# Kernel tuning notes

Measured on AMD Instinct MI355X. Metric: run time of the kernel, lower is better.

## Reference

```python
import jax, jax.numpy as jnp
import numpy as np

B, S, D = 2, 2048, 1024
H, HD = 16, 64

def setup_inputs() -> dict:
    key = jax.random.key(0)
    ks = jax.random.split(key, 5)
    scale = 1.0 / np.sqrt(D)
    x = jax.random.normal(ks[0], (B, S, D), dtype=jnp.float32)
    wq = jax.random.normal(ks[1], (D, H * HD), dtype=jnp.float32) * scale
    wk = jax.random.normal(ks[2], (D, H * HD), dtype=jnp.float32) * scale
    wv = jax.random.normal(ks[3], (D, H * HD), dtype=jnp.float32) * scale
    wo = jax.random.normal(ks[4], (H * HD, D), dtype=jnp.float32) * scale
    zeros = jnp.zeros((H * HD,), dtype=jnp.float32)
    return {"x": x, "wq": wq, "bq": zeros, "wk": wk, "bk": zeros,
            "wv": wv, "bv": zeros, "wo": wo, "bo": jnp.zeros((D,), jnp.float32)}

def reference(x, wq, bq, wk, bk, wv, bv, wo, bo):
    b, s, _ = x.shape
    att_scale = HD ** -0.5
    # QKV projections -> [b, h, s, hd]
    q = (x @ wq + bq).reshape(b, s, H, HD).transpose(0, 2, 1, 3)
    k = (x @ wk + bk).reshape(b, s, H, HD).transpose(0, 2, 1, 3)
    v = (x @ wv + bv).reshape(b, s, H, HD).transpose(0, 2, 1, 3)
    scores = jnp.einsum('bhqd,bhkd->bhqk', q, k) * att_scale
    weights = jax.nn.softmax(scores, axis=-1)
    out = jnp.einsum('bhqk,bhkd->bhqd', weights, v)
    out = out.transpose(0, 2, 1, 3).reshape(b, s, H * HD)
    return out @ wo + bo
```

## Files before the change

### kernel.cpp

```cpp
#include <hip/hip_runtime.h>
#include <hip/hip_bf16.h>

#define B_  2
#define S_  2048
#define D_  1024
#define H_  16
#define HD_ 64
#define M_  (B_*S_)

using bf16x8 = __attribute__((ext_vector_type(8))) short;
using f32x4  = __attribute__((ext_vector_type(4))) float;
using f32x16 = __attribute__((ext_vector_type(16))) float;
using u32x4  = __attribute__((ext_vector_type(4))) unsigned int;
using uint2v = __attribute__((ext_vector_type(2))) unsigned int;

static __device__ __forceinline__ ushort f2bf(float f) {
    __hip_bfloat16 h = __float2bfloat16(f);
    return *reinterpret_cast<ushort*>(&h);
}
static __device__ __forceinline__ float max3f(float a, float b, float c) {
    return fmaxf(fmaxf(a, b), c);
}
static __device__ __forceinline__ float fexp2(float x) {
#if __has_builtin(__builtin_amdgcn_exp2f)
    return __builtin_amdgcn_exp2f(x);
#else
    return exp2f(x);
#endif
}
static __device__ __forceinline__ unsigned int pack_bf16(float p0, float p1) {
    unsigned int a = __float_as_uint(p0), b = __float_as_uint(p1);
    a += 0x7fffu + ((a >> 16) & 1u);
    b += 0x7fffu + ((b >> 16) & 1u);
    return (a >> 16) | (b & 0xffff0000u);
}

#define GLDS16(gp, lp) __builtin_amdgcn_global_load_lds( \
    (const __attribute__((address_space(1))) void*)(gp), \
    (__attribute__((address_space(3))) void*)(lp), 16, 0, 0)

__global__ void convert_f32_bf16(const float* __restrict__ src, ushort* __restrict__ dst, int n) {
    int i = (blockIdx.x * blockDim.x + threadIdx.x) * 4;
    if (i < n) {
        float4 v = *reinterpret_cast<const float4*>(src + i);
        ushort4 o;
        o.x = f2bf(v.x); o.y = f2bf(v.y); o.z = f2bf(v.z); o.w = f2bf(v.w);
        *reinterpret_cast<ushort4*>(dst + i) = o;
    }
}

__global__ void transpose_f32_to_bf16(const float* __restrict__ src, ushort* __restrict__ dst,
                                      int R, int C) {
    __shared__ float t[32][33];
    int c0 = blockIdx.x * 32, r0 = blockIdx.y * 32;
    int tx = threadIdx.x, ty = threadIdx.y;
    #pragma unroll
    for (int i = 0; i < 4; i++)
        t[ty + i*8][tx] = src[(size_t)(r0 + ty + i*8) * C + c0 + tx];
    __syncthreads();
    #pragma unroll
    for (int i = 0; i < 4; i++)
        dst[(size_t)(c0 + ty + i*8) * R + r0 + tx] = f2bf(t[tx][ty + i*8]);
}

__global__ void transpose_v(const ushort* __restrict__ src, ushort* __restrict__ dst) {
    __shared__ ushort t[64][72];
    int bh = blockIdx.y, s0 = blockIdx.x * 64;
    #pragma unroll
    for (int p = 0; p < 2; p++) {
        int idx = threadIdx.x + p * 256;
        int r = idx >> 3, cu = (idx & 7) * 8;
        uint4 v = *reinterpret_cast<const uint4*>(src + (size_t)bh * 131072 + (size_t)(s0 + r) * 64 + cu);
        ushort tmp[8];
        *reinterpret_cast<uint4*>(tmp) = v;
        #pragma unroll
        for (int j = 0; j < 8; j++) t[cu + j][r] = tmp[j];
    }
    __syncthreads();
    #pragma unroll
    for (int p = 0; p < 2; p++) {
        int idx = threadIdx.x + p * 256;
        int r = idx >> 3, cu = (idx & 7) * 8;
        *reinterpret_cast<uint4*>(dst + (size_t)bh * 131072 + (size_t)r * S_ + s0 + cu) =
            *reinterpret_cast<uint4*>(&t[r][cu]);
    }
}

template<int MODE>
__launch_bounds__(256, 2)
__global__ void gemm_bt(const ushort* __restrict__ A, const ushort* __restrict__ Bt,
                        int Mdim, int Ndim, int Kdim,
                        ushort* __restrict__ qout, ushort* __restrict__ kout, ushort* __restrict__ vout,
                        const float* __restrict__ bq, const float* __restrict__ bk, const float* __restrict__ bv,
                        float* __restrict__ out, const float* __restrict__ bias)
{
    __shared__ __align__(16) ushort As[128][32];
    __shared__ __align__(16) ushort Bs[128][32];
    const int tid  = threadIdx.x;
    const int lane = tid & 63, wave = tid >> 6;
    const int wm = wave & 1, wn = wave >> 1;
    const int m0 = blockIdx.y * 128, n0 = blockIdx.x * 128;
    const int g = lane >> 4, c = lane & 15;

    f32x4 acc[4][4];
    #pragma unroll
    for (int i = 0; i < 4; i++)
        #pragma unroll
        for (int j = 0; j < 4; j++) acc[i][j] = (f32x4){0.f, 0.f, 0.f, 0.f};

    const int lrow = lane >> 2;
    const int lcol = (lane & 3) * 8;

    for (int kt = 0; kt < Kdim; kt += 32) {
        #pragma unroll
        for (int p = 0; p < 2; p++) {
            int ch = wave + p * 4;
            GLDS16(A  + (size_t)(m0 + ch*16 + lrow) * Kdim + kt + lcol, &As[ch*16][0]);
            GLDS16(Bt + (size_t)(n0 + ch*16 + lrow) * Kdim + kt + lcol, &Bs[ch*16][0]);
        }
        __syncthreads();
        bf16x8 af[4], bfr[4];
        #pragma unroll
        for (int t = 0; t < 4; t++) {
            af[t]  = *reinterpret_cast<const bf16x8*>(&As[wm*64 + t*16 + c][g*8]);
            bfr[t] = *reinterpret_cast<const bf16x8*>(&Bs[wn*64 + t*16 + c][g*8]);
        }
        #pragma unroll
        for (int i = 0; i < 4; i++)
            #pragma unroll
            for (int j = 0; j < 4; j++)
                acc[i][j] = __builtin_amdgcn_mfma_f32_16x16x32_bf16(af[i], bfr[j], acc[i][j], 0, 0, 0);
        __syncthreads();
    }

    const float qscale = 0.125f * 1.4426950408889634f;
    #pragma unroll
    for (int i = 0; i < 4; i++) {
      #pragma unroll
      for (int j = 0; j < 4; j++) {
        #pragma unroll
        for (int r = 0; r < 4; r++) {
            int row = m0 + wm*64 + i*16 + g*4 + r;
            int col = n0 + wn*64 + j*16 + c;
            float v = acc[i][j][r];
            if (MODE == 0) {
                int which = col >> 10;
                int cc = col & 1023;
                int b = row >> 11, s = row & 2047;
                int h = cc >> 6, hd = cc & 63;
                size_t dst = (((size_t)(b*H_ + h)) * S_ + s) * HD_ + hd;
                if (which == 0)      qout[dst] = f2bf((v + bq[cc]) * qscale);
                else if (which == 1) kout[dst] = f2bf(v + bk[cc]);
                else                 vout[dst] = f2bf(v + bv[cc]);
            } else {
                out[(size_t)row * Ndim + col] = v + bias[col];
            }
        }
      }
    }
}

__launch_bounds__(512, 4)
__global__ void attn_kernel(const ushort* __restrict__ Q, const ushort* __restrict__ K,
                            const ushort* __restrict__ Vt, ushort* __restrict__ O)
{
    __shared__ __align__(16) ushort Ks[2][2][64][64];
    __shared__ __align__(16) ushort Vs[2][2][64][64];
    const int tid = threadIdx.x, lane = tid & 63, w = tid >> 6;
    const int grp = w >> 2, wq4 = w & 3;
    const int q31 = lane & 31, hi = lane >> 5, x7 = lane & 7;

    int lin = blockIdx.x + gridDim.x * blockIdx.y;
    int xcd = lin & 7, idx = lin >> 3;
    int bh = xcd * 4 + (idx & 3);
    int qb = idx >> 2;
    const int q0 = qb * 128;
    const int kt_base = grp * 1024;
    const ushort* Kp = K  + (size_t)bh * S_ * HD_;
    const ushort* Vp = Vt + (size_t)bh * HD_ * S_;

    bf16x8 qf[4];
    #pragma unroll
    for (int c4 = 0; c4 < 4; c4++)
        qf[c4] = *reinterpret_cast<const bf16x8*>(
            Q + (size_t)bh * S_ * HD_ + (size_t)(q0 + wq4*32 + q31) * HD_ + c4*16 + hi*8);

    f32x16 acc0, acc1;
    #pragma unroll
    for (int r = 0; r < 16; r++) { acc0[r] = 0.f; acc1[r] = 0.f; }
    float m_i = -INFINITY, l_i = 0.f;

    const int srow  = lane >> 3;
    const int sslot = (lane & 7) ^ srow;
    const ushort* kg = Kp + (size_t)srow * HD_ + sslot * 8;
    const ushort* vg = Vp + (size_t)srow * S_  + sslot * 8;

    auto stage = [&](int buf, int kt) {
        #pragma unroll
        for (int p = 0; p < 2; p++) {
            int ch = wq4 + p * 4;
            GLDS16(kg + (size_t)(kt + ch*8) * HD_, &Ks[grp][buf][ch*8][0]);
            GLDS16(vg + (size_t)(ch*8) * S_ + kt,  &Vs[grp][buf][ch*8][0]);
        }
    };

    auto softmax_pack = [&](const f32x16& st, bf16x8& pf0, bf16x8& pf1) {
        float g0 = max3f(st[0],  st[1],  st[2]);
        float g1 = max3f(st[3],  st[4],  st[5]);
        float g2 = max3f(st[6],  st[7],  st[8]);
        float g3 = max3f(st[9],  st[10], st[11]);
        float g4 = max3f(st[12], st[13], st[14]);
        float pm = fmaxf(max3f(g0, g1, g2), max3f(g3, g4, st[15]));
#if __has_builtin(__builtin_amdgcn_permlane32_swap)
        {
            uint2v r = __builtin_amdgcn_permlane32_swap(__float_as_uint(pm), __float_as_uint(pm), false, false);
            pm = fmaxf(__uint_as_float(r.x), __uint_as_float(r.y));
        }
#else
        pm = fmaxf(pm, __shfl_xor(pm, 32));
#endif
        if (__any(pm > m_i + 8.f)) {
            float mnew = fmaxf(m_i, pm);
            float al = fexp2(m_i - mnew);
            l_i *= al;
            #pragma unroll
            for (int r = 0; r < 16; r++) { acc0[r] *= al; acc1[r] *= al; }
            m_i = mnew;
        }
        float rs = 0.f;
        unsigned int dd[8];
        #pragma unroll
        for (int r2 = 0; r2 < 8; r2++) {
            float p0 = fexp2(st[r2*2]     - m_i);
            float p1 = fexp2(st[r2*2 + 1] - m_i);
            rs += p0 + p1;
            dd[r2] = pack_bf16(p0, p1);
        }
#if __has_builtin(__builtin_amdgcn_permlane32_swap)
        {
            uint2v r = __builtin_amdgcn_permlane32_swap(__float_as_uint(rs), __float_as_uint(rs), false, false);
            rs = __uint_as_float(r.x) + __uint_as_float(r.y);
        }
#else
        rs += __shfl_xor(rs, 32);
#endif
        l_i += rs;
        u32x4 t0, t1;
#if __has_builtin(__builtin_amdgcn_permlane32_swap)
        {
            uint2v s02 = __builtin_amdgcn_permlane32_swap(dd[0], dd[2], false, false);
            uint2v s13 = __builtin_amdgcn_permlane32_swap(dd[1], dd[3], false, false);
            uint2v s46 = __builtin_amdgcn_permlane32_swap(dd[4], dd[6], false, false);
            uint2v s57 = __builtin_amdgcn_permlane32_swap(dd[5], dd[7], false, false);
            t0 = (u32x4){s02.x, s13.x, s02.y, s13.y};
            t1 = (u32x4){s46.x, s57.x, s46.y, s57.y};
        }
#else
        {
            unsigned int ee[8];
            #pragma unroll
            for (int r2 = 0; r2 < 8; r2++)
                ee[r2] = (unsigned int)__shfl_xor((int)dd[r2], 32);
            t0 = (u32x4){ hi ? ee[2] : dd[0], hi ? ee[3] : dd[1],
                          hi ? dd[2] : ee[0], hi ? dd[3] : ee[1] };
            t1 = (u32x4){ hi ? ee[6] : dd[4], hi ? ee[7] : dd[5],
                          hi ? dd[6] : ee[4], hi ? dd[7] : ee[5] };
        }
#endif
        pf0 = *reinterpret_cast<bf16x8*>(&t0);
        pf1 = *reinterpret_cast<bf16x8*>(&t1);
    };

    auto compute64 = [&](int buf) {
        const ushort (*ks)[64] = Ks[grp][buf];
        const ushort (*vs)[64] = Vs[grp][buf];
        f32x16 st0, st1;
        #pragma unroll
        for (int r = 0; r < 16; r++) { st0[r] = 0.f; st1[r] = 0.f; }
        __builtin_amdgcn_s_setprio(1);
        #pragma unroll
        for (int c4 = 0; c4 < 4; c4++) {
            bf16x8 kf = *reinterpret_cast<const bf16x8*>(&ks[q31][((c4*2 + hi) ^ x7) * 8]);
            st0 = __builtin_amdgcn_mfma_f32_32x32x16_bf16(kf, qf[c4], st0, 0, 0, 0);
        }
        #pragma unroll
        for (int c4 = 0; c4 < 4; c4++) {
            bf16x8 kf = *reinterpret_cast<const bf16x8*>(&ks[32 + q31][((c4*2 + hi) ^ x7) * 8]);
            st1 = __builtin_amdgcn_mfma_f32_32x32x16_bf16(kf, qf[c4], st1, 0, 0, 0);
        }
        __builtin_amdgcn_s_setprio(0);

        bf16x8 pf0, pf1;
        softmax_pack(st0, pf0, pf1);
        {
            bf16x8 vf0 = *reinterpret_cast<const bf16x8*>(&vs[q31]     [((0 + hi) ^ x7) * 8]);
            bf16x8 vf1 = *reinterpret_cast<const bf16x8*>(&vs[q31]     [((2 + hi) ^ x7) * 8]);
            bf16x8 vf2 = *reinterpret_cast<const bf16x8*>(&vs[32 + q31][((0 + hi) ^ x7) * 8]);
            bf16x8 vf3 = *reinterpret_cast<const bf16x8*>(&vs[32 + q31][((2 + hi) ^ x7) * 8]);
            __builtin_amdgcn_s_setprio(1);
            acc0 = __builtin_amdgcn_mfma_f32_32x32x16_bf16(vf0, pf0, acc0, 0, 0, 0);
            acc0 = __builtin_amdgcn_mfma_f32_32x32x16_bf16(vf1, pf1, acc0, 0, 0, 0);
            acc1 = __builtin_amdgcn_mfma_f32_32x32x16_bf16(vf2, pf0, acc1, 0, 0, 0);
            acc1 = __builtin_amdgcn_mfma_f32_32x32x16_bf16(vf3, pf1, acc1, 0, 0, 0);
            __builtin_amdgcn_s_setprio(0);
        }
        softmax_pack(st1, pf0, pf1);
        {
            bf16x8 vf0 = *reinterpret_cast<const bf16x8*>(&vs[q31]     [((4 + hi) ^ x7) * 8]);
            bf16x8 vf1 = *reinterpret_cast<const bf16x8*>(&vs[q31]     [((6 + hi) ^ x7) * 8]);
            bf16x8 vf2 = *reinterpret_cast<const bf16x8*>(&vs[32 + q31][((4 + hi) ^ x7) * 8]);
            bf16x8 vf3 = *reinterpret_cast<const bf16x8*>(&vs[32 + q31][((6 + hi) ^ x7) * 8]);
            __builtin_amdgcn_s_setprio(1);
            acc0 = __builtin_amdgcn_mfma_f32_32x32x16_bf16(vf0, pf0, acc0, 0, 0, 0);
            acc0 = __builtin_amdgcn_mfma_f32_32x32x16_bf16(vf1, pf1, acc0, 0, 0, 0);
            acc1 = __builtin_amdgcn_mfma_f32_32x32x16_bf16(vf2, pf0, acc1, 0, 0, 0);
            acc1 = __builtin_amdgcn_mfma_f32_32x32x16_bf16(vf3, pf1, acc1, 0, 0, 0);
            __builtin_amdgcn_s_setprio(0);
        }
    };

    stage(0, kt_base);
    __syncthreads();
    #pragma unroll 1
    for (int it = 0; it < 15; ++it) {
        stage((it & 1) ^ 1, kt_base + (it + 1) * 64);
        compute64(it & 1);
        __syncthreads();
    }
    compute64(1);

    __syncthreads();
    float* fb = (wq4 < 2) ? reinterpret_cast<float*>(&Ks[0][0][0][0])
                          : reinterpret_cast<float*>(&Vs[0][0][0][0]);
    const int slot = ((wq4 & 1) * 64 + lane) * 35;
    if (grp == 1) {
        #pragma unroll
        for (int r = 0; r < 16; r++) { fb[slot + r] = acc0[r]; fb[slot + 16 + r] = acc1[r]; }
        fb[slot + 32] = m_i;
        fb[slot + 33] = l_i;
    }
    __syncthreads();
    if (grp == 0) {
        float m2 = fb[slot + 32], l2 = fb[slot + 33];
        float mm = fmaxf(m_i, m2);
        float a1 = fexp2(m_i - mm), a2 = fexp2(m2 - mm);
        float inv = 1.f / (l_i * a1 + l2 * a2);
        const int b = bh >> 4, h = bh & 15;
        const int s = q0 + wq4*32 + q31;
        ushort* op = O + (size_t)(b*S_ + s) * 1024 + h*64;
        #pragma unroll
        for (int rg = 0; rg < 4; rg++) {
            int hd0 = rg*8 + hi*4;
            ushort4 o;
            o.x = f2bf((acc0[rg*4+0]*a1 + fb[slot + rg*4+0]*a2) * inv);
            o.y = f2bf((acc0[rg*4+1]*a1 + fb[slot + rg*4+1]*a2) * inv);
            o.z = f2bf((acc0[rg*4+2]*a1 + fb[slot + rg*4+2]*a2) * inv);
            o.w = f2bf((acc0[rg*4+3]*a1 + fb[slot + rg*4+3]*a2) * inv);
            *reinterpret_cast<ushort4*>(op + hd0) = o;
            o.x = f2bf((acc1[rg*4+0]*a1 + fb[slot + 16 + rg*4+0]*a2) * inv);
            o.y = f2bf((acc1[rg*4+1]*a1 + fb[slot + 16 + rg*4+1]*a2) * inv);
            o.z = f2bf((acc1[rg*4+2]*a1 + fb[slot + 16 + rg*4+2]*a2) * inv);
            o.w = f2bf((acc1[rg*4+3]*a1 + fb[slot + 16 + rg*4+3]*a2) * inv);
            *reinterpret_cast<ushort4*>(op + 32 + hd0) = o;
        }
    }
}

extern "C" void kernel_launch(void* const* d_in, const int* in_sizes, int n_in,
                              void* d_out, int out_size, void* d_ws, size_t ws_size,
                              hipStream_t stream)
{
    const float* x  = (const float*)d_in[0];
    const float* wq = (const float*)d_in[1];
    const float* bq = (const float*)d_in[2];
    const float* wk = (const float*)d_in[3];
    const float* bk = (const float*)d_in[4];
    const float* wv = (const float*)d_in[5];
    const float* bv = (const float*)d_in[6];
    const float* wo = (const float*)d_in[7];
    const float* bo = (const float*)d_in[8];
    float* out = (float*)d_out;

    char* ws = (char*)d_ws;
    ushort* xb    = (ushort*)(ws);
    ushort* wqkvT = (ushort*)(ws + (8ull  << 20));
    ushort* woT   = (ushort*)(ws + (14ull << 20));
    ushort* qw    = (ushort*)(ws + (16ull << 20));
    ushort* kw    = (ushort*)(ws + (24ull << 20));
    ushort* vw    = (ushort*)(ws + (32ull << 20));
    ushort* ao    = (ushort*)(ws + (40ull << 20));
    ushort* vtw   = xb;

    convert_f32_bf16<<<4096, 256, 0, stream>>>(x, xb, M_ * D_);
    dim3 tb(32, 8);
    transpose_f32_to_bf16<<<dim3(32, 32), tb, 0, stream>>>(wq, wqkvT,               1024, 1024);
    transpose_f32_to_bf16<<<dim3(32, 32), tb, 0, stream>>>(wk, wqkvT + 1024*1024,   1024, 1024);
    transpose_f32_to_bf16<<<dim3(32, 32), tb, 0, stream>>>(wv, wqkvT + 2*1024*1024, 1024, 1024);
    transpose_f32_to_bf16<<<dim3(32, 32), tb, 0, stream>>>(wo, woT,                 1024, 1024);

    gemm_bt<0><<<dim3(24, 32), 256, 0, stream>>>(xb, wqkvT, M_, 3072, 1024,
                                                 qw, kw, vw, bq, bk, bv, nullptr, nullptr);
    transpose_v<<<dim3(32, 32), 256, 0, stream>>>(vw, vtw);
    attn_kernel<<<dim3(16, 32), 512, 0, stream>>>(qw, kw, vtw, ao);
    gemm_bt<1><<<dim3(8, 32), 256, 0, stream>>>(ao, woT, M_, 1024, 1024,
                                                nullptr, nullptr, nullptr, nullptr, nullptr, nullptr,
                                                out, bo);
}
```

Before: 225.8 us.

## Double-buffer GEMM LDS tiles with BK=64, XOR swizzle, and merge weight transposes

The bf16 GEMM main loop now uses two LDS buffers with a K-tile of 64, issuing global-to-LDS loads for the next tile before computing on the current one. This halves the number of barriers per K and overlaps memory latency with MFMA work. The LDS layout is XOR-swizzled by row to avoid bank conflicts on the wider 64-element rows. Separately, the four weight transpose launches are merged into one launch with a z-dimension, which removes launch overhead. LDS use grows to 64KB per block, which may limit occupancy at the two-blocks-per-CU launch bound.

```diff
diff --git a/kernel.cpp b/kernel.cpp
--- a/kernel.cpp
+++ b/kernel.cpp
@@ -49,8 +49,13 @@
     }
 }
 
-__global__ void transpose_f32_to_bf16(const float* __restrict__ src, ushort* __restrict__ dst,
-                                      int R, int C) {
+__global__ void transpose_w4(const float* __restrict__ wq, const float* __restrict__ wk,
+                             const float* __restrict__ wv, const float* __restrict__ wo,
+                             ushort* __restrict__ wqkvT, ushort* __restrict__ woT) {
+    const int z = blockIdx.z;
+    const float* src = (z == 0) ? wq : (z == 1) ? wk : (z == 2) ? wv : wo;
+    ushort* dst = (z < 3) ? (wqkvT + (size_t)z * 1024 * 1024) : woT;
+    const int R = 1024, C = 1024;
     __shared__ float t[32][33];
     int c0 = blockIdx.x * 32, r0 = blockIdx.y * 32;
     int tx = threadIdx.x, ty = threadIdx.y;
@@ -94,8 +99,8 @@
                         const float* __restrict__ bq, const float* __restrict__ bk, const float* __restrict__ bv,
                         float* __restrict__ out, const float* __restrict__ bias)
 {
-    __shared__ __align__(16) ushort As[128][32];
-    __shared__ __align__(16) ushort Bs[128][32];
+    __shared__ __align__(16) ushort As[2][128][64];
+    __shared__ __align__(16) ushort Bs[2][128][64];
     const int tid  = threadIdx.x;
     const int lane = tid & 63, wave = tid >> 6;
     const int wm = wave & 1, wn = wave >> 1;
@@ -108,30 +113,48 @@
         #pragma unroll
         for (int j = 0; j < 4; j++) acc[i][j] = (f32x4){0.f, 0.f, 0.f, 0.f};
 
-    const int lrow = lane >> 2;
-    const int lcol = (lane & 3) * 8;
-
-    for (int kt = 0; kt < Kdim; kt += 32) {
-        #pragma unroll
-        for (int p = 0; p < 2; p++) {
+    const int arow  = lane >> 3;
+    const int aslot = (lane & 7) ^ arow;
+    const ushort* Ag = A  + (size_t)(m0 + arow) * Kdim + aslot * 8;
+    const ushort* Bg = Bt + (size_t)(n0 + arow) * Kdim + aslot * 8;
+
+    auto stage = [&](int buf, int kt) {
+        #pragma unroll
+        for (int p = 0; p < 4; p++) {
             int ch = wave + p * 4;
-            GLDS16(A  + (size_t)(m0 + ch*16 + lrow) * Kdim + kt + lcol, &As[ch*16][0]);
-            GLDS16(Bt + (size_t)(n0 + ch*16 + lrow) * Kdim + kt + lcol, &Bs[ch*16][0]);
-        }
+            GLDS16(Ag + (size_t)(ch*8) * Kdim + kt, &As[buf][ch*8][0]);
+            GLDS16(Bg + (size_t)(ch*8) * Kdim + kt, &Bs[buf][ch*8][0]);
+        }
+    };
+
+    auto compute = [&](int buf) {
+        #pragma unroll
+        for (int ks = 0; ks < 2; ks++) {
+            bf16x8 af[4], bfr[4];
+            #pragma unroll
+            for (int t = 0; t < 4; t++) {
+                int sl = ((ks*4 + g) ^ (c & 7)) * 8;
+                af[t]  = *reinterpret_cast<const bf16x8*>(&As[buf][wm*64 + t*16 + c][sl]);
+                bfr[t] = *reinterpret_cast<const bf16x8*>(&Bs[buf][wn*64 + t*16 + c][sl]);
+            }
+            #pragma unroll
+            for (int i = 0; i < 4; i++)
+                #pragma unroll
+                for (int j = 0; j < 4; j++)
+                    acc[i][j] = __builtin_amdgcn_mfma_f32_16x16x32_bf16(af[i], bfr[j], acc[i][j], 0, 0, 0);
+        }
+    };
+
+    const int NT = Kdim >> 6;
+    stage(0, 0);
+    __syncthreads();
+    #pragma unroll 1
+    for (int it = 0; it < NT - 1; ++it) {
+        stage((it + 1) & 1, (it + 1) * 64);
+        compute(it & 1);
         __syncthreads();
-        bf16x8 af[4], bfr[4];
-        #pragma unroll
-        for (int t = 0; t < 4; t++) {
-            af[t]  = *reinterpret_cast<const bf16x8*>(&As[wm*64 + t*16 + c][g*8]);
-            bfr[t] = *reinterpret_cast<const bf16x8*>(&Bs[wn*64 + t*16 + c][g*8]);
-        }
-        #pragma unroll
-        for (int i = 0; i < 4; i++)
-            #pragma unroll
-            for (int j = 0; j < 4; j++)
-                acc[i][j] = __builtin_amdgcn_mfma_f32_16x16x32_bf16(af[i], bfr[j], acc[i][j], 0, 0, 0);
-        __syncthreads();
-    }
+    }
+    compute((NT - 1) & 1);
 
     const float qscale = 0.125f * 1.4426950408889634f;
     #pragma unroll
@@ -392,11 +415,7 @@
     ushort* vtw   = xb;
 
     convert_f32_bf16<<<4096, 256, 0, stream>>>(x, xb, M_ * D_);
-    dim3 tb(32, 8);
-    transpose_f32_to_bf16<<<dim3(32, 32), tb, 0, stream>>>(wq, wqkvT,               1024, 1024);
-    transpose_f32_to_bf16<<<dim3(32, 32), tb, 0, stream>>>(wk, wqkvT + 1024*1024,   1024, 1024);
-    transpose_f32_to_bf16<<<dim3(32, 32), tb, 0, stream>>>(wv, wqkvT + 2*1024*1024, 1024, 1024);
-    transpose_f32_to_bf16<<<dim3(32, 32), tb, 0, stream>>>(wo, woT,                 1024, 1024);
+    transpose_w4<<<dim3(32, 32, 4), dim3(32, 8), 0, stream>>>(wq, wk, wv, wo, wqkvT, woT);
 
     gemm_bt<0><<<dim3(24, 32), 256, 0, stream>>>(xb, wqkvT, M_, 3072, 1024,
                                                  qw, kw, vw, bq, bk, bv, nullptr, nullptr);
```

Result: slower. 232.3 us (+2.9%).
